# Optimization experiments

Hardware: AMD Instinct MI355X
Metric: run time of the kernel (lower is better)

The kernel has to match this reference:

```python
import jax, jax.numpy as jnp
import numpy as np

N, P, C_IN, C_OUT, C_FEAT = 100000, 32, 4, 64, 9
BN_EPS = 1e-3


def setup_inputs() -> dict:
    key = jax.random.key(0)
    k1, k2, k3, k4 = jax.random.split(key, 4)
    voxels = jax.random.normal(k1, (N, P, C_IN), dtype=jnp.float32)
    num_points_per_voxel = jax.random.randint(k2, (N,), 1, P + 1, dtype=jnp.int32)
    voxel_centers = jax.random.normal(k3, (N, 2), dtype=jnp.float32)
    W = jax.random.normal(k4, (C_OUT, C_FEAT), dtype=jnp.float32) * (1.0 / np.sqrt(C_FEAT))
    gamma = jnp.ones((C_OUT,), dtype=jnp.float32)
    beta = jnp.zeros((C_OUT,), dtype=jnp.float32)
    return {"voxels": voxels, "num_points_per_voxel": num_points_per_voxel,
            "voxel_centers": voxel_centers, "W": W, "gamma": gamma, "beta": beta}


def reference(voxels, num_points_per_voxel, voxel_centers, W, gamma, beta):
    npts = num_points_per_voxel.astype(voxels.dtype)[:, None, None]  # [N,1,1]
    # cluster offset: per-pillar mean of xyz
    points_mean = voxels[:, :, :3].sum(axis=1, keepdims=True) / npts  # [N,1,3]
    f_cluster = voxels[:, :, :3] - points_mean                        # [N,P,3]
    # center offset: xy minus Cartesian voxel center
    f_center = voxels[:, :, :2] - voxel_centers[:, None, :]           # [N,P,2]
    features = jnp.concatenate([voxels, f_cluster, f_center], axis=-1)  # [N,P,9]
    # zero out padded points
    mask = num_points_per_voxel[:, None] > jnp.arange(P, dtype=jnp.int32)[None, :]
    features = features * mask[:, :, None].astype(features.dtype)
    # PFNLayer (last_layer=True): linear(no bias) -> BN(batch stats) -> relu -> max over points
    x = jnp.einsum('npc,oc->npo', features, W)  # [N,P,64]
    mean = x.mean(axis=(0, 1))
    var = ((x - mean) ** 2).mean(axis=(0, 1))   # biased var, as torch BN training
    x = (x - mean) * jax.lax.rsqrt(var + BN_EPS) * gamma + beta
    x = jax.nn.relu(x)
    return x.max(axis=1)  # [N,64]
```

## Files before the change

kernel.cpp:

```cpp
#include <hip/hip_runtime.h>
#include <math.h>

#define N_PILLARS 100000
#define P_PTS 32
#define BN_EPS 1e-3f

typedef short v8s __attribute__((ext_vector_type(8)));
typedef float v16f __attribute__((ext_vector_type(16)));

__device__ __forceinline__ unsigned short f2bf(float f) {
    unsigned int u = __float_as_uint(f);
    return (unsigned short)((u + 0x8000u) >> 16);
}
__device__ __forceinline__ float bcast(float v, int sl) {
    return __int_as_float(__builtin_amdgcn_readlane(__float_as_int(v), sl));
}

__global__ __launch_bounds__(256, 2) void pfn_main(
    const float* __restrict__ vox,
    const int*   __restrict__ npts,
    const float* __restrict__ ctr,
    const float* __restrict__ W,
    float*       __restrict__ gsums,
    float*       __restrict__ out)
{
    __shared__ float red[2][4][64];
    const int tid = threadIdx.x, wave = tid >> 6, lane = tid & 63;
    const int col = lane & 31;
    const bool blo = (lane < 32);

    v8s Bs0 = {0,0,0,0,0,0,0,0};
    v8s Bs1 = Bs0, Bm0 = Bs0, Bm1 = Bs0;
    float tw0[5], tw1[5];
    {
        const int c0 = col, c1 = 32 + col;
        float wb0[4], wb1[4];
        wb0[0] = W[c0*9+0] + W[c0*9+4] + W[c0*9+7];
        wb0[1] = W[c0*9+1] + W[c0*9+5] + W[c0*9+8];
        wb0[2] = W[c0*9+2] + W[c0*9+6];
        wb0[3] = W[c0*9+3];
        wb1[0] = W[c1*9+0] + W[c1*9+4] + W[c1*9+7];
        wb1[1] = W[c1*9+1] + W[c1*9+5] + W[c1*9+8];
        wb1[2] = W[c1*9+2] + W[c1*9+6];
        wb1[3] = W[c1*9+3];
#pragma unroll
        for (int j = 0; j < 5; ++j) { tw0[j] = W[c0*9+4+j]; tw1[j] = W[c1*9+4+j]; }
        if (blo) {
#pragma unroll
            for (int j = 0; j < 4; ++j) {
                Bs0[j] = (short)f2bf(wb0[j]); Bm0[j] = Bs0[j];
                Bs1[j] = (short)f2bf(wb1[j]); Bm1[j] = Bs1[j];
            }
            Bm0[4] = (short)f2bf(-1e30f);
            Bm1[4] = (short)f2bf(-1e30f);
        }
    }

    float accS1 = 0.f, accS2 = 0.f;
    const int wid = blockIdx.x * 4 + wave, nw = gridDim.x * 4;
    for (int n = wid; n < N_PILLARS; n += nw) {
        const int np = npts[n];
        float4 pt = make_float4(0.f, 0.f, 0.f, 0.f);
        if (blo) pt = ((const float4*)(vox + (size_t)n * 128))[col];
        const float cx = ctr[n*2], cy = ctr[n*2+1];

        const bool valid = blo && (col < np);
        v8s A = {0,0,0,0,0,0,0,0};
        A[0] = valid ? (short)f2bf(pt.x) : (short)0;
        A[1] = valid ? (short)f2bf(pt.y) : (short)0;
        A[2] = valid ? (short)f2bf(pt.z) : (short)0;
        A[3] = valid ? (short)f2bf(pt.w) : (short)0;
        A[4] = (blo && col >= np) ? (short)0x3F80 : (short)0;

        float sx = pt.x, sy = pt.y, sz = pt.z;
#pragma unroll
        for (int m = 1; m < 32; m <<= 1) {
            sx += __shfl_xor(sx, m); sy += __shfl_xor(sy, m); sz += __shfl_xor(sz, m);
        }
        const float inv = 1.f / (float)np;
        const float mx = bcast(sx,0)*inv, my = bcast(sy,0)*inv, mz = bcast(sz,0)*inv;

        v16f z;
#pragma unroll
        for (int r = 0; r < 16; ++r) z[r] = 0.f;
        v16f Ds0 = __builtin_amdgcn_mfma_f32_32x32x16_bf16(A, Bs0, z, 0, 0, 0);
        v16f Dm0 = __builtin_amdgcn_mfma_f32_32x32x16_bf16(A, Bm0, z, 0, 0, 0);
        v16f Ds1 = __builtin_amdgcn_mfma_f32_32x32x16_bf16(A, Bs1, z, 0, 0, 0);
        v16f Dm1 = __builtin_amdgcn_mfma_f32_32x32x16_bf16(A, Bm1, z, 0, 0, 0);

        const float t0 = -(mx*tw0[0] + my*tw0[1] + mz*tw0[2] + cx*tw0[3] + cy*tw0[4]);
        const float t1 = -(mx*tw1[0] + my*tw1[1] + mz*tw1[2] + cx*tw1[3] + cy*tw1[4]);
        const float npf = (float)np;

        float s10 = 0.f, s20 = 0.f, h0 = -INFINITY;
        float s11 = 0.f, s21 = 0.f, h1 = -INFINITY;
#pragma unroll
        for (int r = 0; r < 16; ++r) {
            s10 += Ds0[r]; s20 = fmaf(Ds0[r], Ds0[r], s20); h0 = fmaxf(h0, Dm0[r]);
            s11 += Ds1[r]; s21 = fmaf(Ds1[r], Ds1[r], s21); h1 = fmaxf(h1, Dm1[r]);
        }
        s10 += __shfl_xor(s10, 32); s20 += __shfl_xor(s20, 32);
        s11 += __shfl_xor(s11, 32); s21 += __shfl_xor(s21, 32);
        h0 = fmaxf(h0, __shfl_xor(h0, 32));
        h1 = fmaxf(h1, __shfl_xor(h1, 32));

        const float S1_0 = s10 + npf * t0;
        const float S2_0 = s20 + t0 * fmaf(2.f, s10, npf * t0);
        const float S1_1 = s11 + npf * t1;
        const float S2_1 = s21 + t1 * fmaf(2.f, s11, npf * t1);
        float H0 = h0 + t0, H1 = h1 + t1;
        if (np < P_PTS) { H0 = fmaxf(H0, 0.f); H1 = fmaxf(H1, 0.f); }

        accS1 += blo ? S1_0 : S1_1;
        accS2 += blo ? S2_0 : S2_1;
        out[(size_t)n * 64 + lane] = blo ? H0 : H1;
    }

    red[0][wave][lane] = accS1;
    red[1][wave][lane] = accS2;
    __syncthreads();
    if (wave == 0) {
        float a = red[0][0][lane] + red[0][1][lane] + red[0][2][lane] + red[0][3][lane];
        float b = red[1][0][lane] + red[1][1][lane] + red[1][2][lane] + red[1][3][lane];
        atomicAdd(&gsums[lane], a);
        atomicAdd(&gsums[64 + lane], b);
    }
}

__global__ __launch_bounds__(256) void pfn_finish(
    const float* __restrict__ gsums,
    const float* __restrict__ gamma,
    const float* __restrict__ beta,
    float*       __restrict__ out)
{
    const int g = blockIdx.x * 256 + threadIdx.x;
    const int ch0 = (g * 4) & 63;
    const float invNP = 1.f / (float)(N_PILLARS * P_PTS);
    float sc[4], bs[4];
#pragma unroll
    for (int j = 0; j < 4; ++j) {
        const int ch = ch0 + j;
        const float mean = gsums[ch] * invNP;
        const float var  = gsums[64 + ch] * invNP - mean * mean;
        const float s    = gamma[ch] * rsqrtf(var + BN_EPS);
        sc[j] = s;
        bs[j] = beta[ch] - mean * s;
    }
    const int total4 = N_PILLARS * 16;
    const int stride = gridDim.x * 256;
    for (int i = g; i < total4; i += stride) {
        float4 v = ((float4*)out)[i];
        v.x = fmaxf(0.f, fmaf(v.x, sc[0], bs[0]));
        v.y = fmaxf(0.f, fmaf(v.y, sc[1], bs[1]));
        v.z = fmaxf(0.f, fmaf(v.z, sc[2], bs[2]));
        v.w = fmaxf(0.f, fmaf(v.w, sc[3], bs[3]));
        ((float4*)out)[i] = v;
    }
}

extern "C" void kernel_launch(void* const* d_in, const int* in_sizes, int n_in,
                              void* d_out, int out_size, void* d_ws, size_t ws_size,
                              hipStream_t stream) {
    const float* voxels  = (const float*)d_in[0];
    const int*   npts    = (const int*)d_in[1];
    const float* centers = (const float*)d_in[2];
    const float* W       = (const float*)d_in[3];
    const float* gamma   = (const float*)d_in[4];
    const float* beta    = (const float*)d_in[5];
    float* out = (float*)d_out;

    float* gsums = (float*)d_ws;

    hipMemsetAsync(d_ws, 0, 512, stream);
    pfn_main<<<2048, 256, 0, stream>>>(voxels, npts, centers, W, gsums, out);
    pfn_finish<<<1024, 256, 0, stream>>>(gsums, gamma, beta, out);
}
```

Baseline: 167.8 us.

## Compute BN stats from 9x9 feature moments, apply BN in the max pass

Splits the work into a stats kernel and a max kernel. The stats kernel accumulates first and second moments of the 9 input features (9 sums plus 45 cross products) per pillar pair, using all 64 lanes. BN mean and variance per channel are then derived algebraically from W and these moments. The max kernel applies the BN affine and ReLU directly, which removes the separate finish pass over the output and the per-pillar sum MFMAs. The cost is that the voxels are read twice, along with extra per-pillar means traffic and 54 accumulator registers per thread. Variance computed from raw moments may also be less numerically stable.

```diff
diff --git a/kernel.cpp b/kernel.cpp
--- a/kernel.cpp
+++ b/kernel.cpp
@@ -2,6 +2,7 @@
 #include <math.h>
 
 #define N_PILLARS 100000
+#define N_PAIRS   (N_PILLARS / 2)
 #define P_PTS 32
 #define BN_EPS 1e-3f
 
@@ -12,149 +13,179 @@
     unsigned int u = __float_as_uint(f);
     return (unsigned short)((u + 0x8000u) >> 16);
 }
-__device__ __forceinline__ float bcast(float v, int sl) {
-    return __int_as_float(__builtin_amdgcn_readlane(__float_as_int(v), sl));
-}
-
-__global__ __launch_bounds__(256, 2) void pfn_main(
+
+
+__global__ __launch_bounds__(256, 4) void pfn_stats(
     const float* __restrict__ vox,
     const int*   __restrict__ npts,
     const float* __restrict__ ctr,
-    const float* __restrict__ W,
-    float*       __restrict__ gsums,
-    float*       __restrict__ out)
+    float*       __restrict__ gstats,
+    float4*      __restrict__ means)
 {
-    __shared__ float red[2][4][64];
+    __shared__ float smem[4][54];
+    const int tid = threadIdx.x, wave = tid >> 6, lane = tid & 63;
+    const int pl = lane & 31, half = lane >> 5;
+
+    float F[9], M[45];
+#pragma unroll
+    for (int j = 0; j < 9; ++j) F[j] = 0.f;
+#pragma unroll
+    for (int j = 0; j < 45; ++j) M[j] = 0.f;
+
+    const int wid = blockIdx.x * 4 + wave, nw = gridDim.x * 4;
+    for (int pr = wid; pr < N_PAIRS; pr += nw) {
+        const int n0 = pr * 2;
+        const float4 pt = ((const float4*)(vox + (size_t)n0 * 128))[lane];
+        const int2   np2 = ((const int2*)npts)[pr];
+        const float4 c4  = ((const float4*)ctr)[pr];
+        const int   np  = half ? np2.y : np2.x;
+        const float cx  = half ? c4.z : c4.x;
+        const float cy  = half ? c4.w : c4.y;
+
+        float sx = pt.x, sy = pt.y, sz = pt.z;
+#pragma unroll
+        for (int m = 1; m <= 16; m <<= 1) {
+            sx += __shfl_xor(sx, m); sy += __shfl_xor(sy, m); sz += __shfl_xor(sz, m);
+        }
+        const float inv = 1.f / (float)np;
+        const float mx = sx * inv, my = sy * inv, mz = sz * inv;
+        if (pl == 0)
+            means[n0 + half] = make_float4(mx, my, mz, (float)np);
+
+        const bool valid = pl < np;
+        float f[9];
+        f[0] = valid ? pt.x : 0.f;
+        f[1] = valid ? pt.y : 0.f;
+        f[2] = valid ? pt.z : 0.f;
+        f[3] = valid ? pt.w : 0.f;
+        f[4] = valid ? (pt.x - mx) : 0.f;
+        f[5] = valid ? (pt.y - my) : 0.f;
+        f[6] = valid ? (pt.z - mz) : 0.f;
+        f[7] = valid ? (pt.x - cx) : 0.f;
+        f[8] = valid ? (pt.y - cy) : 0.f;
+
+#pragma unroll
+        for (int j = 0; j < 9; ++j) F[j] += f[j];
+        int idx = 0;
+#pragma unroll
+        for (int k = 0; k < 9; ++k)
+#pragma unroll
+            for (int j = k; j < 9; ++j) { M[idx] = fmaf(f[k], f[j], M[idx]); ++idx; }
+    }
+
+#pragma unroll
+    for (int j = 0; j < 9; ++j)
+#pragma unroll
+        for (int m = 1; m < 64; m <<= 1) F[j] += __shfl_xor(F[j], m);
+#pragma unroll
+    for (int j = 0; j < 45; ++j)
+#pragma unroll
+        for (int m = 1; m < 64; m <<= 1) M[j] += __shfl_xor(M[j], m);
+
+    if (lane == 0) {
+#pragma unroll
+        for (int j = 0; j < 9; ++j)  smem[wave][j]     = F[j];
+#pragma unroll
+        for (int j = 0; j < 45; ++j) smem[wave][9 + j] = M[j];
+    }
+    __syncthreads();
+    if (tid < 54) {
+        const float v = smem[0][tid] + smem[1][tid] + smem[2][tid] + smem[3][tid];
+        atomicAdd(&gstats[tid], v);
+    }
+}
+
+__global__ __launch_bounds__(256, 4) void pfn_max(
+    const float*  __restrict__ vox,
+    const int*    __restrict__ npts,
+    const float*  __restrict__ ctr,
+    const float*  __restrict__ W,
+    const float*  __restrict__ gstats,
+    const float*  __restrict__ gamma,
+    const float*  __restrict__ beta,
+    const float4* __restrict__ means,
+    float*        __restrict__ out)
+{
     const int tid = threadIdx.x, wave = tid >> 6, lane = tid & 63;
     const int col = lane & 31;
     const bool blo = (lane < 32);
-
-    v8s Bs0 = {0,0,0,0,0,0,0,0};
-    v8s Bs1 = Bs0, Bm0 = Bs0, Bm1 = Bs0;
-    float tw0[5], tw1[5];
+    const int ch = lane;
+
+    float Wr[9];
+#pragma unroll
+    for (int j = 0; j < 9; ++j) Wr[j] = W[ch * 9 + j];
+
+    const float invNP = 1.f / (float)(N_PILLARS * P_PTS);
+    float mean = 0.f;
+#pragma unroll
+    for (int j = 0; j < 9; ++j) mean = fmaf(Wr[j], gstats[j], mean);
+    mean *= invNP;
+    float q = 0.f;
     {
+        int idx = 0;
+#pragma unroll
+        for (int k = 0; k < 9; ++k)
+#pragma unroll
+            for (int j = k; j < 9; ++j) {
+                const float coef = (j == k) ? 1.f : 2.f;
+                q = fmaf(coef * Wr[k] * Wr[j], gstats[9 + idx], q);
+                ++idx;
+            }
+    }
+    const float var = q * invNP - mean * mean;
+    const float sc  = gamma[ch] * rsqrtf(var + BN_EPS);
+    const float bs  = beta[ch] - mean * sc;
+
+    v8s Bm0 = {0,0,0,0,0,0,0,0}, Bm1 = Bm0;
+    if (blo) {
         const int c0 = col, c1 = 32 + col;
-        float wb0[4], wb1[4];
-        wb0[0] = W[c0*9+0] + W[c0*9+4] + W[c0*9+7];
-        wb0[1] = W[c0*9+1] + W[c0*9+5] + W[c0*9+8];
-        wb0[2] = W[c0*9+2] + W[c0*9+6];
-        wb0[3] = W[c0*9+3];
-        wb1[0] = W[c1*9+0] + W[c1*9+4] + W[c1*9+7];
-        wb1[1] = W[c1*9+1] + W[c1*9+5] + W[c1*9+8];
-        wb1[2] = W[c1*9+2] + W[c1*9+6];
-        wb1[3] = W[c1*9+3];
-#pragma unroll
-        for (int j = 0; j < 5; ++j) { tw0[j] = W[c0*9+4+j]; tw1[j] = W[c1*9+4+j]; }
-        if (blo) {
-#pragma unroll
-            for (int j = 0; j < 4; ++j) {
-                Bs0[j] = (short)f2bf(wb0[j]); Bm0[j] = Bs0[j];
-                Bs1[j] = (short)f2bf(wb1[j]); Bm1[j] = Bs1[j];
-            }
-            Bm0[4] = (short)f2bf(-1e30f);
-            Bm1[4] = (short)f2bf(-1e30f);
-        }
-    }
-
-    float accS1 = 0.f, accS2 = 0.f;
+        Bm0[0] = (short)f2bf(W[c0*9+0] + W[c0*9+4] + W[c0*9+7]);
+        Bm0[1] = (short)f2bf(W[c0*9+1] + W[c0*9+5] + W[c0*9+8]);
+        Bm0[2] = (short)f2bf(W[c0*9+2] + W[c0*9+6]);
+        Bm0[3] = (short)f2bf(W[c0*9+3]);
+        Bm0[4] = (short)f2bf(-1e30f);
+        Bm1[0] = (short)f2bf(W[c1*9+0] + W[c1*9+4] + W[c1*9+7]);
+        Bm1[1] = (short)f2bf(W[c1*9+1] + W[c1*9+5] + W[c1*9+8]);
+        Bm1[2] = (short)f2bf(W[c1*9+2] + W[c1*9+6]);
+        Bm1[3] = (short)f2bf(W[c1*9+3]);
+        Bm1[4] = (short)f2bf(-1e30f);
+    }
+
+    v16f z;
+#pragma unroll
+    for (int r = 0; r < 16; ++r) z[r] = 0.f;
+
     const int wid = blockIdx.x * 4 + wave, nw = gridDim.x * 4;
     for (int n = wid; n < N_PILLARS; n += nw) {
         const int np = npts[n];
         float4 pt = make_float4(0.f, 0.f, 0.f, 0.f);
         if (blo) pt = ((const float4*)(vox + (size_t)n * 128))[col];
-        const float cx = ctr[n*2], cy = ctr[n*2+1];
-
-        const bool valid = blo && (col < np);
+        const float4 m = means[n];
+        const float2 c = ((const float2*)ctr)[n];
+
         v8s A = {0,0,0,0,0,0,0,0};
-        A[0] = valid ? (short)f2bf(pt.x) : (short)0;
-        A[1] = valid ? (short)f2bf(pt.y) : (short)0;
-        A[2] = valid ? (short)f2bf(pt.z) : (short)0;
-        A[3] = valid ? (short)f2bf(pt.w) : (short)0;
+        A[0] = (short)f2bf(pt.x); A[1] = (short)f2bf(pt.y);
+        A[2] = (short)f2bf(pt.z); A[3] = (short)f2bf(pt.w);
         A[4] = (blo && col >= np) ? (short)0x3F80 : (short)0;
 
-        float sx = pt.x, sy = pt.y, sz = pt.z;
-#pragma unroll
-        for (int m = 1; m < 32; m <<= 1) {
-            sx += __shfl_xor(sx, m); sy += __shfl_xor(sy, m); sz += __shfl_xor(sz, m);
+        const v16f Dm0 = __builtin_amdgcn_mfma_f32_32x32x16_bf16(A, Bm0, z, 0, 0, 0);
+        const v16f Dm1 = __builtin_amdgcn_mfma_f32_32x32x16_bf16(A, Bm1, z, 0, 0, 0);
+
+        const float t = -(m.x*Wr[4] + m.y*Wr[5] + m.z*Wr[6] + c.x*Wr[7] + c.y*Wr[8]);
+
+        float h0 = Dm0[0], h1 = Dm1[0];
+#pragma unroll
+        for (int r = 1; r < 16; ++r) {
+            h0 = fmaxf(h0, Dm0[r]);
+            h1 = fmaxf(h1, Dm1[r]);
         }
-        const float inv = 1.f / (float)np;
-        const float mx = bcast(sx,0)*inv, my = bcast(sy,0)*inv, mz = bcast(sz,0)*inv;
-
-        v16f z;
-#pragma unroll
-        for (int r = 0; r < 16; ++r) z[r] = 0.f;
-        v16f Ds0 = __builtin_amdgcn_mfma_f32_32x32x16_bf16(A, Bs0, z, 0, 0, 0);
-        v16f Dm0 = __builtin_amdgcn_mfma_f32_32x32x16_bf16(A, Bm0, z, 0, 0, 0);
-        v16f Ds1 = __builtin_amdgcn_mfma_f32_32x32x16_bf16(A, Bs1, z, 0, 0, 0);
-        v16f Dm1 = __builtin_amdgcn_mfma_f32_32x32x16_bf16(A, Bm1, z, 0, 0, 0);
-
-        const float t0 = -(mx*tw0[0] + my*tw0[1] + mz*tw0[2] + cx*tw0[3] + cy*tw0[4]);
-        const float t1 = -(mx*tw1[0] + my*tw1[1] + mz*tw1[2] + cx*tw1[3] + cy*tw1[4]);
-        const float npf = (float)np;
-
-        float s10 = 0.f, s20 = 0.f, h0 = -INFINITY;
-        float s11 = 0.f, s21 = 0.f, h1 = -INFINITY;
-#pragma unroll
-        for (int r = 0; r < 16; ++r) {
-            s10 += Ds0[r]; s20 = fmaf(Ds0[r], Ds0[r], s20); h0 = fmaxf(h0, Dm0[r]);
-            s11 += Ds1[r]; s21 = fmaf(Ds1[r], Ds1[r], s21); h1 = fmaxf(h1, Dm1[r]);
-        }
-        s10 += __shfl_xor(s10, 32); s20 += __shfl_xor(s20, 32);
-        s11 += __shfl_xor(s11, 32); s21 += __shfl_xor(s21, 32);
         h0 = fmaxf(h0, __shfl_xor(h0, 32));
         h1 = fmaxf(h1, __shfl_xor(h1, 32));
 
-        const float S1_0 = s10 + npf * t0;
-        const float S2_0 = s20 + t0 * fmaf(2.f, s10, npf * t0);
-        const float S1_1 = s11 + npf * t1;
-        const float S2_1 = s21 + t1 * fmaf(2.f, s11, npf * t1);
-        float H0 = h0 + t0, H1 = h1 + t1;
-        if (np < P_PTS) { H0 = fmaxf(H0, 0.f); H1 = fmaxf(H1, 0.f); }
-
-        accS1 += blo ? S1_0 : S1_1;
-        accS2 += blo ? S2_0 : S2_1;
-        out[(size_t)n * 64 + lane] = blo ? H0 : H1;
-    }
-
-    red[0][wave][lane] = accS1;
-    red[1][wave][lane] = accS2;
-    __syncthreads();
-    if (wave == 0) {
-        float a = red[0][0][lane] + red[0][1][lane] + red[0][2][lane] + red[0][3][lane];
-        float b = red[1][0][lane] + red[1][1][lane] + red[1][2][lane] + red[1][3][lane];
-        atomicAdd(&gsums[lane], a);
-        atomicAdd(&gsums[64 + lane], b);
-    }
-}
-
-__global__ __launch_bounds__(256) void pfn_finish(
-    const float* __restrict__ gsums,
-    const float* __restrict__ gamma,
-    const float* __restrict__ beta,
-    float*       __restrict__ out)
-{
-    const int g = blockIdx.x * 256 + threadIdx.x;
-    const int ch0 = (g * 4) & 63;
-    const float invNP = 1.f / (float)(N_PILLARS * P_PTS);
-    float sc[4], bs[4];
-#pragma unroll
-    for (int j = 0; j < 4; ++j) {
-        const int ch = ch0 + j;
-        const float mean = gsums[ch] * invNP;
-        const float var  = gsums[64 + ch] * invNP - mean * mean;
-        const float s    = gamma[ch] * rsqrtf(var + BN_EPS);
-        sc[j] = s;
-        bs[j] = beta[ch] - mean * s;
-    }
-    const int total4 = N_PILLARS * 16;
-    const int stride = gridDim.x * 256;
-    for (int i = g; i < total4; i += stride) {
-        float4 v = ((float4*)out)[i];
-        v.x = fmaxf(0.f, fmaf(v.x, sc[0], bs[0]));
-        v.y = fmaxf(0.f, fmaf(v.y, sc[1], bs[1]));
-        v.z = fmaxf(0.f, fmaf(v.z, sc[2], bs[2]));
-        v.w = fmaxf(0.f, fmaf(v.w, sc[3], bs[3]));
-        ((float4*)out)[i] = v;
+        float H = (blo ? h0 : h1) + t;
+        if (np < P_PTS) H = fmaxf(H, 0.f);
+
+        out[(size_t)n * 64 + ch] = fmaxf(0.f, fmaf(H, sc, bs));
     }
 }
 
@@ -169,9 +200,10 @@
     const float* beta    = (const float*)d_in[5];
     float* out = (float*)d_out;
 
-    float* gsums = (float*)d_ws;
-
-    hipMemsetAsync(d_ws, 0, 512, stream);
-    pfn_main<<<2048, 256, 0, stream>>>(voxels, npts, centers, W, gsums, out);
-    pfn_finish<<<1024, 256, 0, stream>>>(gsums, gamma, beta, out);
-}
+    float*  gstats = (float*)d_ws;
+    float4* means  = (float4*)((char*)d_ws + 1024);
+
+    hipMemsetAsync(d_ws, 0, 256, stream);
+    pfn_stats<<<2048, 256, 0, stream>>>(voxels, npts, centers, gstats, means);
+    pfn_max<<<2048, 256, 0, stream>>>(voxels, npts, centers, W, gstats, gamma, beta, means, out);
+}
```

New measurement: 173.9 us. 3.6% more time.
